# Kernel optimization log

Measured on AMD Instinct MI355X. Metric: run time of the kernel, lower is better.

Reference implementation:

```python
import jax, jax.numpy as jnp
import numpy as np

N_NODES = 50000
N_EDGES = 800000
IN_DIM = 256
HID = 64
LAT = 64
HEADS = 4
NUM_GRAPHS = 64
NEG_SLOPE = 0.2


def _gat_layer(h_in, src, dst, W, a_s, a_d, b, heads, concat):
    N = h_in.shape[0]
    F_ = W.shape[1] // heads
    h = (h_in @ W).reshape(N, heads, F_)              # [N,H,F]
    al_s = jnp.sum(h * a_s, axis=-1)                  # [N,H]
    al_d = jnp.sum(h * a_d, axis=-1)                  # [N,H]
    e = jax.nn.leaky_relu(al_s[src] + al_d[dst], NEG_SLOPE)  # [E,H]
    # scatter-softmax over edges grouped by destination node
    m = jax.ops.segment_max(e, dst, num_segments=N)
    e = jnp.exp(e - m[dst])
    s = jax.ops.segment_sum(e, dst, num_segments=N)
    alpha = e / (s[dst] + 1e-16)                      # [E,H]
    out = jax.ops.segment_sum(h[src] * alpha[:, :, None], dst, num_segments=N)
    out = out.reshape(N, heads * F_) if concat else out.mean(axis=1)
    return out + b


def setup_inputs() -> dict:
    key = jax.random.key(0)
    ks = jax.random.split(key, 20)
    g = lambda k, shp, sc: jax.random.normal(k, shp, jnp.float32) * sc
    inp = {}
    inp['x'] = g(ks[0], (N_NODES, IN_DIM), 1.0)
    inp['edge_index'] = jax.random.randint(ks[1], (2, N_EDGES), 0, N_NODES, jnp.int32)
    inp['batch'] = jnp.sort(jax.random.randint(ks[2], (N_NODES,), 0, NUM_GRAPHS, jnp.int32))
    # layer 0: IN_DIM -> HID, 4 heads, concat
    inp['W1'] = g(ks[3], (IN_DIM, HEADS * HID), 0.05)
    inp['a1s'] = g(ks[4], (HEADS, HID), 0.05)
    inp['a1d'] = g(ks[5], (HEADS, HID), 0.05)
    inp['b1'] = jnp.zeros((HEADS * HID,), jnp.float32)
    # layer 1: 4*HID -> HID, 4 heads, concat
    inp['W2'] = g(ks[6], (HEADS * HID, HEADS * HID), 0.05)
    inp['a2s'] = g(ks[7], (HEADS, HID), 0.05)
    inp['a2d'] = g(ks[8], (HEADS, HID), 0.05)
    inp['b2'] = jnp.zeros((HEADS * HID,), jnp.float32)
    # layer 2: 4*HID -> LAT, 1 head, mean
    inp['W3'] = g(ks[9], (HEADS * HID, LAT), 0.05)
    inp['a3s'] = g(ks[10], (1, LAT), 0.05)
    inp['a3d'] = g(ks[11], (1, LAT), 0.05)
    inp['b3'] = jnp.zeros((LAT,), jnp.float32)
    # VAE head
    inp['Wmu'] = g(ks[12], (LAT, LAT), 0.1)
    inp['bmu'] = jnp.zeros((LAT,), jnp.float32)
    inp['Wlv'] = g(ks[13], (LAT, LAT), 0.1)
    inp['blv'] = jnp.zeros((LAT,), jnp.float32)
    return inp


def reference(x, edge_index, batch, W1, a1s, a1d, b1, W2, a2s, a2d, b2,
              W3, a3s, a3d, b3, Wmu, bmu, Wlv, blv):
    N = x.shape[0]
    loop = jnp.arange(N, dtype=edge_index.dtype)
    src = jnp.concatenate([edge_index[0], loop])   # add self-loops (PyG default)
    dst = jnp.concatenate([edge_index[1], loop])
    h = _gat_layer(x, src, dst, W1, a1s, a1d, b1, HEADS, True)
    h = jax.nn.elu(h)
    h = _gat_layer(h, src, dst, W2, a2s, a2d, b2, HEADS, True)
    h = jax.nn.elu(h)
    h = _gat_layer(h, src, dst, W3, a3s, a3d, b3, 1, False)
    # global mean pool per graph
    sums = jax.ops.segment_sum(h, batch, num_segments=NUM_GRAPHS)
    cnts = jax.ops.segment_sum(jnp.ones((N,), h.dtype), batch, num_segments=NUM_GRAPHS)
    pooled = sums / jnp.maximum(cnts, 1.0)[:, None]  # [G, LAT]
    mu = pooled @ Wmu + bmu
    logvar = pooled @ Wlv + blv
    std = jnp.exp(0.5 * logvar)
    eps = jax.random.normal(jax.random.key(42), std.shape, std.dtype)
    z = mu + eps * std
    return (mu, logvar, z)
```

## Files before the change

kernel.cpp:

```cpp
#include <hip/hip_runtime.h>
#include <hip/hip_bf16.h>
#include <cstdint>
#include <math.h>


#define N_NODES 50000
#define N_EDGES 800000
#define NEG_SLOPE 0.2f
#define CAP 128
#define WTB 192

typedef __hip_bfloat16 bf16;
typedef short short8 __attribute__((ext_vector_type(8)));
typedef float floatx4 __attribute__((ext_vector_type(4)));
typedef float floatx2 __attribute__((ext_vector_type(2)));

__device__ __forceinline__ float bf2f(bf16 v){ return __bfloat162float(v); }
__device__ __forceinline__ float bflo(unsigned u){ union{unsigned u; float f;} c; c.u = u<<16; return c.f; }
__device__ __forceinline__ float bfhi(unsigned u){ union{unsigned u; float f;} c; c.u = u & 0xFFFF0000u; return c.f; }
__device__ __forceinline__ float leaky(float v){ return v>0.f ? v : NEG_SLOPE*v; }
__device__ __forceinline__ unsigned short f2bu(float f){
  union{ bf16 b; unsigned short u; } c; c.b = __float2bfloat16(f); return c.u;
}
__device__ __forceinline__ unsigned char f2fp8(float v){
  int p = __builtin_amdgcn_cvt_pk_fp8_f32(v, v, 0, false);
  return (unsigned char)(p & 0xff);
}
__device__ __forceinline__ void acc_fp8x4(float* acc, unsigned wrd, float wgt){
  floatx2 lo = __builtin_amdgcn_cvt_pk_f32_fp8((int)wrd, false);
  floatx2 hi = __builtin_amdgcn_cvt_pk_f32_fp8((int)wrd, true);
  acc[0] = fmaf(lo[0], wgt, acc[0]);
  acc[1] = fmaf(lo[1], wgt, acc[1]);
  acc[2] = fmaf(hi[0], wgt, acc[2]);
  acc[3] = fmaf(hi[1], wgt, acc[3]);
}

__device__ __forceinline__ void tf_round(unsigned& x0, unsigned& x1, int r){
  x0 += x1; x1 = (x1<<r)|(x1>>(32-r)); x1 ^= x0;
}
__device__ __forceinline__ void threefry2x32(unsigned k0, unsigned k1, unsigned& x0, unsigned& x1){
  unsigned ks2 = k0 ^ k1 ^ 0x1BD11BDAu;
  x0 += k0; x1 += k1;
  tf_round(x0,x1,13); tf_round(x0,x1,15); tf_round(x0,x1,26); tf_round(x0,x1,6);
  x0 += k1; x1 += ks2 + 1u;
  tf_round(x0,x1,17); tf_round(x0,x1,29); tf_round(x0,x1,16); tf_round(x0,x1,24);
  x0 += ks2; x1 += k0 + 2u;
  tf_round(x0,x1,13); tf_round(x0,x1,15); tf_round(x0,x1,26); tf_round(x0,x1,6);
  x0 += k0; x1 += k1 + 3u;
  tf_round(x0,x1,17); tf_round(x0,x1,29); tf_round(x0,x1,16); tf_round(x0,x1,24);
  x0 += k1; x1 += ks2 + 4u;
  tf_round(x0,x1,13); tf_round(x0,x1,15); tf_round(x0,x1,26); tf_round(x0,x1,6);
  x0 += ks2; x1 += k0 + 5u;
}

__device__ __forceinline__ float erfinv_approx(float x){
  float w = -log1pf(-x*x);
  float p;
  if (w < 5.0f){
    w = w - 2.5f;
    p = 2.81022636e-08f;
    p = fmaf(p,w,3.43273939e-07f);
    p = fmaf(p,w,-3.5233877e-06f);
    p = fmaf(p,w,-4.39150654e-06f);
    p = fmaf(p,w,0.00021858087f);
    p = fmaf(p,w,-0.00125372503f);
    p = fmaf(p,w,-0.00417768164f);
    p = fmaf(p,w,0.246640727f);
    p = fmaf(p,w,1.50140941f);
  } else {
    w = sqrtf(w) - 3.0f;
    p = -0.000200214257f;
    p = fmaf(p,w,0.000100950558f);
    p = fmaf(p,w,0.00134934322f);
    p = fmaf(p,w,-0.00367342844f);
    p = fmaf(p,w,0.00573950773f);
    p = fmaf(p,w,-0.0076224613f);
    p = fmaf(p,w,0.00943887047f);
    p = fmaf(p,w,1.00167406f);
    p = fmaf(p,w,2.83297682f);
  }
  return p*x;
}

__global__ __launch_bounds__(256) void wt_build_kernel(
        const float* __restrict__ W1, const float* __restrict__ W2,
        const float* __restrict__ W3, short* __restrict__ Wt1,
        short* __restrict__ Wt2, short* __restrict__ Wt3,
        const int* __restrict__ ei, int* __restrict__ deg,
        unsigned short* __restrict__ csr){
  __shared__ float tile[32][33];
  const int bx = (int)blockIdx.x;
  if (bx < WTB){
    const int z = bx >> 6, rem = bx & 63;
    const int gx = rem & 7, gy = rem >> 3;
    const float* W; short* Wt; int Nn;
    if (z == 0){ W = W1; Wt = Wt1; Nn = 256; }
    else if (z == 1){ W = W2; Wt = Wt2; Nn = 256; }
    else { W = W3; Wt = Wt3; Nn = 64; }
    const int n0 = gx*32, k0 = gy*32;
    if (n0 >= Nn) return;
    const int tx = threadIdx.x & 31, ty = threadIdx.x >> 5;
    #pragma unroll
    for (int i=0;i<4;++i)
      tile[ty+8*i][tx] = W[(size_t)(k0+ty+8*i)*Nn + n0 + tx];
    __syncthreads();
    #pragma unroll
    for (int i=0;i<4;++i)
      Wt[(size_t)(n0+ty+8*i)*256 + k0 + tx] = (short)f2bu(tile[tx][ty+8*i]);
  } else {
    int idx = (bx - WTB)*256 + (int)threadIdx.x;
    if (idx < N_EDGES + N_NODES){
      int s_ = (idx < N_EDGES) ? ei[idx]          : idx - N_EDGES;
      int d_ = (idx < N_EDGES) ? ei[N_EDGES+idx]  : idx - N_EDGES;
      int r = atomicAdd(&deg[d_], 1);
      if (r < CAP) csr[(size_t)d_*CAP + r] = (unsigned short)s_;
    }
  }
}

template<int OUT, bool INBF>
__global__ __launch_bounds__(256) void gemm_mfma_kernel(const void* __restrict__ inp,
        const short* __restrict__ Wt, void* __restrict__ outv,
        const float* __restrict__ a_s, const float* __restrict__ a_d,
        float* __restrict__ als, float* __restrict__ ald, int N){
  constexpr int M_BLK = (OUT==256) ? 64 : 256;
  constexpr int H = (OUT==256) ? 4 : 1;
  __shared__ short As[M_BLK*48];
  __shared__ short Bs[OUT*48];
  const int t = threadIdx.x;
  const int w = t>>6, lane = t&63;
  const int lm = lane&15, g = lane>>4;
  const int m0 = blockIdx.x * M_BLK;
  const int m_off = (OUT==256) ? 0 : w*64;
  const int n0    = (OUT==256) ? w*64 : 0;

  floatx4 acc[4][4] = {};

  for (int kk=0; kk<8; ++kk){
    const int k0 = kk*32;
    __syncthreads();
    for (int a = t; a < M_BLK*4; a += 256){
      int r = a>>2, c = a&3;
      int gr = m0 + r;
      uint4 v = make_uint4(0u,0u,0u,0u);
      if (gr < N){
        if constexpr (INBF){
          v = *(const uint4*)((const bf16*)inp + (size_t)gr*256 + k0 + c*8);
        } else {
          const float* p = (const float*)inp + (size_t)gr*256 + k0 + c*8;
          float4 f0 = *(const float4*)p;
          float4 f1 = *(const float4*)(p+4);
          v.x = (unsigned)f2bu(f0.x) | ((unsigned)f2bu(f0.y)<<16);
          v.y = (unsigned)f2bu(f0.z) | ((unsigned)f2bu(f0.w)<<16);
          v.z = (unsigned)f2bu(f1.x) | ((unsigned)f2bu(f1.y)<<16);
          v.w = (unsigned)f2bu(f1.z) | ((unsigned)f2bu(f1.w)<<16);
        }
      }
      *(uint4*)&As[r*48 + c*8] = v;
    }
    for (int a = t; a < OUT*4; a += 256){
      int r = a>>2, c = a&3;
      uint4 v = *(const uint4*)(Wt + (size_t)r*256 + k0 + c*8);
      *(uint4*)&Bs[r*48 + c*8] = v;
    }
    __syncthreads();
    short8 af[4], bfr[4];
    #pragma unroll
    for (int mt=0;mt<4;++mt)
      af[mt] = *(const short8*)&As[(m_off + mt*16 + lm)*48 + g*8];
    #pragma unroll
    for (int nt=0;nt<4;++nt)
      bfr[nt] = *(const short8*)&Bs[(n0 + nt*16 + lm)*48 + g*8];
    #pragma unroll
    for (int mt=0;mt<4;++mt)
      #pragma unroll
      for (int nt=0;nt<4;++nt)
        acc[mt][nt] = __builtin_amdgcn_mfma_f32_16x16x32_bf16(af[mt], bfr[nt], acc[mt][nt], 0, 0, 0);
  }

  float asv[4], adv[4];
  #pragma unroll
  for (int nt=0;nt<4;++nt){
    asv[nt] = a_s[n0 + nt*16 + lm];
    adv[nt] = a_d[n0 + nt*16 + lm];
  }
  const int head = (OUT==256) ? w : 0;
  #pragma unroll
  for (int mt=0;mt<4;++mt){
    #pragma unroll
    for (int reg=0;reg<4;++reg){
      int gr = m0 + m_off + mt*16 + g*4 + reg;
      bool valid = gr < N;
      float ps = 0.f, pd = 0.f;
      #pragma unroll
      for (int nt=0;nt<4;++nt){
        float v = acc[mt][nt][reg];
        if (valid){
          ((unsigned char*)outv)[(size_t)gr*OUT + n0 + nt*16 + lm] = f2fp8(v);
        }
        ps = fmaf(v, asv[nt], ps);
        pd = fmaf(v, adv[nt], pd);
      }
      #pragma unroll
      for (int o=1;o<16;o<<=1){ ps += __shfl_xor(ps,o); pd += __shfl_xor(pd,o); }
      if (lm==0 && valid){
        als[gr*H + head] = ps;
        ald[gr*H + head] = pd;
      }
    }
  }
}

template<bool ELU>
__global__ __launch_bounds__(256) void aggregate4_kernel(const unsigned char* __restrict__ h8,
        const float* __restrict__ als, const float* __restrict__ ald,
        const int* __restrict__ deg, const unsigned short* __restrict__ csr,
        const float* __restrict__ bias, bf16* __restrict__ out){
  __shared__ int   s_src[4][64];
  __shared__ float s_w[4][64][4];
  const int wv_ = threadIdx.x >> 6;
  const int n = blockIdx.x*4 + wv_;
  if (n >= N_NODES) return;
  const int lane = threadIdx.x & 63;
  const int r = lane>>4;
  const int f = lane&15;
  const int head = f>>2;
  const int p0 = n*CAP;
  const int cnt = min(deg[n], CAP);
  const float4 aldn4 = *(const float4*)(ald + n*4);
  float ssum = 0.f;
  float acc[16] = {};
  for (int c=0; c<cnt; c+=64){
    int e = c + lane;
    int src = n; float4 w4 = make_float4(0.f,0.f,0.f,0.f);
    if (e < cnt){
      src = (int)csr[p0+e];
      float4 av = *(const float4*)(als + src*4);
      w4.x = expf(leaky(av.x + aldn4.x));
      w4.y = expf(leaky(av.y + aldn4.y));
      w4.z = expf(leaky(av.z + aldn4.z));
      w4.w = expf(leaky(av.w + aldn4.w));
    }
    s_src[wv_][lane] = src;
    *(float4*)&s_w[wv_][lane][0] = w4;
    int ce = min(64, cnt - c);
    int cp = (ce+7)&~7;
    for (int i=0;i<cp;i+=8){
      int src0 = s_src[wv_][i+r], src1 = s_src[wv_][i+4+r];
      float w0 = s_w[wv_][i+r][head], w1 = s_w[wv_][i+4+r][head];
      uint4 h0 = *(const uint4*)(h8 + (size_t)src0*256 + f*16);
      uint4 h1 = *(const uint4*)(h8 + (size_t)src1*256 + f*16);
      ssum += w0 + w1;
      acc_fp8x4(acc+0,  h0.x, w0); acc_fp8x4(acc+4,  h0.y, w0);
      acc_fp8x4(acc+8,  h0.z, w0); acc_fp8x4(acc+12, h0.w, w0);
      acc_fp8x4(acc+0,  h1.x, w1); acc_fp8x4(acc+4,  h1.y, w1);
      acc_fp8x4(acc+8,  h1.z, w1); acc_fp8x4(acc+12, h1.w, w1);
    }
  }
  #pragma unroll
  for (int j=0;j<16;++j){
    acc[j] += __shfl_xor(acc[j], 16);
    acc[j] += __shfl_xor(acc[j], 32);
  }
  ssum += __shfl_xor(ssum, 16);
  ssum += __shfl_xor(ssum, 32);
  if (r==0){
    float inv = 1.f/(ssum + 1e-16f);
    #pragma unroll
    for (int half=0; half<2; ++half){
      float4 b0 = *(const float4*)(bias + f*16 + half*8);
      float4 b1 = *(const float4*)(bias + f*16 + half*8 + 4);
      float rv[8];
      rv[0]=acc[half*8+0]*inv+b0.x; rv[1]=acc[half*8+1]*inv+b0.y;
      rv[2]=acc[half*8+2]*inv+b0.z; rv[3]=acc[half*8+3]*inv+b0.w;
      rv[4]=acc[half*8+4]*inv+b1.x; rv[5]=acc[half*8+5]*inv+b1.y;
      rv[6]=acc[half*8+6]*inv+b1.z; rv[7]=acc[half*8+7]*inv+b1.w;
      union{ bf16 b[8]; uint4 u; } pk;
      #pragma unroll
      for (int j=0;j<8;++j){
        float v = rv[j];
        if (ELU) v = (v>0.f)?v:expm1f(v);
        pk.b[j] = __float2bfloat16(v);
      }
      *(uint4*)(out + (size_t)n*256 + f*16 + half*8) = pk.u;
    }
  }
}

__global__ __launch_bounds__(256) void aggregate1_kernel(const unsigned char* __restrict__ h8,
        const float* __restrict__ als, const float* __restrict__ ald,
        const int* __restrict__ deg, const unsigned short* __restrict__ csr,
        const float* __restrict__ bias, bf16* __restrict__ out){
  __shared__ int   s_src[4][64];
  __shared__ float s_w[4][64];
  const int wv_ = threadIdx.x >> 6;
  const int n = blockIdx.x*4 + wv_;
  if (n >= N_NODES) return;
  const int lane = threadIdx.x & 63;
  const int r = lane>>4;
  const int f = lane&15;
  const int p0 = n*CAP;
  const int cnt = min(deg[n], CAP);
  const float aldn = ald[n];
  float ssum = 0.f;
  float acc[4] = {};
  for (int c=0; c<cnt; c+=64){
    int e = c + lane;
    int src = n; float wv = 0.f;
    if (e < cnt){
      src = (int)csr[p0+e];
      wv = expf(leaky(als[src] + aldn));
    }
    s_src[wv_][lane] = src; s_w[wv_][lane] = wv;
    int ce = min(64, cnt - c);
    int cp = (ce+7)&~7;
    for (int i=0;i<cp;i+=8){
      int src0 = s_src[wv_][i+r], src1 = s_src[wv_][i+4+r];
      float w0 = s_w[wv_][i+r],   w1 = s_w[wv_][i+4+r];
      unsigned h0 = *(const unsigned*)(h8 + (size_t)src0*64 + f*4);
      unsigned h1 = *(const unsigned*)(h8 + (size_t)src1*64 + f*4);
      ssum += w0 + w1;
      acc_fp8x4(acc, h0, w0);
      acc_fp8x4(acc, h1, w1);
    }
  }
  #pragma unroll
  for (int j=0;j<4;++j){
    acc[j] += __shfl_xor(acc[j], 16);
    acc[j] += __shfl_xor(acc[j], 32);
  }
  ssum += __shfl_xor(ssum, 16);
  ssum += __shfl_xor(ssum, 32);
  if (r==0){
    float inv = 1.f/(ssum + 1e-16f);
    union{ bf16 b[4]; uint2 u; } pk;
    #pragma unroll
    for (int j=0;j<4;++j) pk.b[j] = __float2bfloat16(acc[j]*inv + bias[f*4+j]);
    *(uint2*)(out + (size_t)n*64 + f*4) = pk.u;
  }
}

__global__ __launch_bounds__(64) void pool_kernel(const bf16* __restrict__ h3,
        const int* __restrict__ batch, float* __restrict__ psum, float* __restrict__ pcnt,
        int N, int chunk){
  int n0 = blockIdx.x*chunk;
  if (n0 >= N) return;
  int n1 = min(N, n0+chunk);
  int t = threadIdx.x;
  int gcur = batch[n0];
  float acc = 0.f, cnt = 0.f;
  for (int n=n0; n<n1; ++n){
    int g = batch[n];
    if (g != gcur){
      atomicAdd(&psum[gcur*64+t], acc);
      if (t==0) atomicAdd(&pcnt[gcur], cnt);
      acc = 0.f; cnt = 0.f; gcur = g;
    }
    acc += bf2f(h3[(size_t)n*64+t]);
    cnt += 1.f;
  }
  atomicAdd(&psum[gcur*64+t], acc);
  if (t==0) atomicAdd(&pcnt[gcur], cnt);
}

__global__ __launch_bounds__(64) void head_kernel(const float* __restrict__ psum,
        const float* __restrict__ pcnt,
        const float* __restrict__ Wmu, const float* __restrict__ bmu,
        const float* __restrict__ Wlv, const float* __restrict__ blv,
        float* __restrict__ out){
  int g = blockIdx.x, t = threadIdx.x;
  __shared__ float p[64];
  float cnt = fmaxf(pcnt[g], 1.0f);
  p[t] = psum[g*64+t] / cnt;
  __syncthreads();
  float mu = bmu[t], lv = blv[t];
  for (int k=0;k<64;++k){
    float pk = p[k];
    mu = fmaf(pk, Wmu[(size_t)k*64+t], mu);
    lv = fmaf(pk, Wlv[(size_t)k*64+t], lv);
  }
  int i = g*64 + t;
  unsigned x0 = 0u, x1 = (unsigned)i;
  threefry2x32(0u, 42u, x0, x1);
  unsigned bits = x0 ^ x1;
  float f = __uint_as_float((bits>>9) | 0x3F800000u) - 1.0f;
  const float lo = __uint_as_float(0xBF7FFFFFu);
  float u = fmaxf(lo, f*2.0f + lo);
  float eps = 1.41421356f * erfinv_approx(u);
  float z = mu + eps * expf(0.5f*lv);
  out[i]        = mu;
  out[4096 + i] = lv;
  out[8192 + i] = z;
}

extern "C" void kernel_launch(void* const* d_in, const int* in_sizes, int n_in,
                              void* d_out, int out_size, void* d_ws, size_t ws_size,
                              hipStream_t stream){
  const float* x    = (const float*)d_in[0];
  const int*   ei   = (const int*)d_in[1];
  const int*   batch= (const int*)d_in[2];
  const float* W1   = (const float*)d_in[3];
  const float* a1s  = (const float*)d_in[4];
  const float* a1d  = (const float*)d_in[5];
  const float* b1   = (const float*)d_in[6];
  const float* W2   = (const float*)d_in[7];
  const float* a2s  = (const float*)d_in[8];
  const float* a2d  = (const float*)d_in[9];
  const float* b2   = (const float*)d_in[10];
  const float* W3   = (const float*)d_in[11];
  const float* a3s  = (const float*)d_in[12];
  const float* a3d  = (const float*)d_in[13];
  const float* b3   = (const float*)d_in[14];
  const float* Wmu  = (const float*)d_in[15];
  const float* bmu  = (const float*)d_in[16];
  const float* Wlv  = (const float*)d_in[17];
  const float* blv  = (const float*)d_in[18];
  float* out = (float*)d_out;

  const int N = N_NODES, E = N_EDGES;
  const int ET = E + N;

  char* ws = (char*)d_ws;
  size_t o = 0;
  auto alloc = [&](size_t bytes)->void*{
    void* p = ws + o; o += (bytes + 255) & ~(size_t)255; return p;
  };
  bf16*  hA      = (bf16*) alloc((size_t)N*256*2);
  unsigned char* hB8 = (unsigned char*)alloc((size_t)N*256);
  unsigned char* h38 = (unsigned char*)alloc((size_t)N*64);
  float* als     = (float*)alloc((size_t)N*4*4);
  float* ald     = (float*)alloc((size_t)N*4*4);
  const size_t degBytes  = ((size_t)N*4 + 255) & ~(size_t)255;
  const size_t poolBytes = 64*64*4 + 64*4;
  int*   deg     = (int*)  alloc((size_t)N*4);
  float* psum    = (float*)alloc(poolBytes);
  float* pcnt    = psum + 64*64;
  unsigned short* csr16 = (unsigned short*)alloc((size_t)N*CAP*2);
  short* Wt1     = (short*)alloc(256*256*2);
  short* Wt2     = (short*)alloc(256*256*2);
  short* Wt3     = (short*)alloc(64*256*2);
  (void)ws_size; (void)n_in; (void)in_sizes; (void)out_size;

  hipMemsetAsync(deg, 0, degBytes + poolBytes, stream);

  const int buildBlocks = (ET + 255)/256;
  wt_build_kernel<<<WTB + buildBlocks, 256, 0, stream>>>(
      W1, W2, W3, Wt1, Wt2, Wt3, ei, deg, csr16);

  gemm_mfma_kernel<256,false><<<(N+63)/64, 256, 0, stream>>>(x, Wt1, hB8, a1s, a1d, als, ald, N);
  aggregate4_kernel<true><<<(N+3)/4, 256, 0, stream>>>(hB8, als, ald, deg, csr16, b1, hA);

  gemm_mfma_kernel<256,true><<<(N+63)/64, 256, 0, stream>>>(hA, Wt2, hB8, a2s, a2d, als, ald, N);
  aggregate4_kernel<true><<<(N+3)/4, 256, 0, stream>>>(hB8, als, ald, deg, csr16, b2, hA);

  gemm_mfma_kernel<64,true><<<(N+255)/256, 256, 0, stream>>>(hA, Wt3, h38, a3s, a3d, als, ald, N);
  aggregate1_kernel<<<(N+3)/4, 256, 0, stream>>>(h38, als, ald, deg, csr16, b3, hA);

  const int PBLK = 512;
  const int chunk = (N + PBLK - 1)/PBLK;
  pool_kernel<<<PBLK, 64, 0, stream>>>(hA, batch, psum, pcnt, N, chunk);
  head_kernel<<<64, 64, 0, stream>>>(psum, pcnt, Wmu, bmu, Wlv, blv, out);
}
```

Baseline: 417.9 us.

## Fuse layer-1 GEMM with CSR build into one launch; split weight transpose

```diff
diff --git a/kernel.cpp b/kernel.cpp
--- a/kernel.cpp
+++ b/kernel.cpp
@@ -8,7 +8,7 @@
 #define N_EDGES 800000
 #define NEG_SLOPE 0.2f
 #define CAP 128
-#define WTB 192
+#define GB1 ((N_NODES+63)/64)
 
 typedef __hip_bfloat16 bf16;
 typedef short short8 __attribute__((ext_vector_type(8)));
@@ -82,38 +82,113 @@
   return p*x;
 }
 
-__global__ __launch_bounds__(256) void wt_build_kernel(
+__global__ __launch_bounds__(256) void wt_all_kernel(
         const float* __restrict__ W1, const float* __restrict__ W2,
         const float* __restrict__ W3, short* __restrict__ Wt1,
-        short* __restrict__ Wt2, short* __restrict__ Wt3,
+        short* __restrict__ Wt2, short* __restrict__ Wt3){
+  const float* W; short* Wt; int Nn;
+  if (blockIdx.z == 0){ W = W1; Wt = Wt1; Nn = 256; }
+  else if (blockIdx.z == 1){ W = W2; Wt = Wt2; Nn = 256; }
+  else { W = W3; Wt = Wt3; Nn = 64; }
+  const int n0 = blockIdx.x*32, k0 = blockIdx.y*32;
+  if (n0 >= Nn) return;
+  __shared__ float tile[32][33];
+  const int tx = threadIdx.x & 31, ty = threadIdx.x >> 5;
+  #pragma unroll
+  for (int i=0;i<4;++i)
+    tile[ty+8*i][tx] = W[(size_t)(k0+ty+8*i)*Nn + n0 + tx];
+  __syncthreads();
+  #pragma unroll
+  for (int i=0;i<4;++i)
+    Wt[(size_t)(n0+ty+8*i)*256 + k0 + tx] = (short)f2bu(tile[tx][ty+8*i]);
+}
+
+__global__ __launch_bounds__(256) void fused_g1b_kernel(
+        const float* __restrict__ x, const short* __restrict__ Wt1,
+        unsigned char* __restrict__ hB8,
+        const float* __restrict__ a1s, const float* __restrict__ a1d,
+        float* __restrict__ als, float* __restrict__ ald,
         const int* __restrict__ ei, int* __restrict__ deg,
         unsigned short* __restrict__ csr){
-  __shared__ float tile[32][33];
+  __shared__ short As[64*48];
   const int bx = (int)blockIdx.x;
-  if (bx < WTB){
-    const int z = bx >> 6, rem = bx & 63;
-    const int gx = rem & 7, gy = rem >> 3;
-    const float* W; short* Wt; int Nn;
-    if (z == 0){ W = W1; Wt = Wt1; Nn = 256; }
-    else if (z == 1){ W = W2; Wt = Wt2; Nn = 256; }
-    else { W = W3; Wt = Wt3; Nn = 64; }
-    const int n0 = gx*32, k0 = gy*32;
-    if (n0 >= Nn) return;
-    const int tx = threadIdx.x & 31, ty = threadIdx.x >> 5;
-    #pragma unroll
-    for (int i=0;i<4;++i)
-      tile[ty+8*i][tx] = W[(size_t)(k0+ty+8*i)*Nn + n0 + tx];
-    __syncthreads();
-    #pragma unroll
-    for (int i=0;i<4;++i)
-      Wt[(size_t)(n0+ty+8*i)*256 + k0 + tx] = (short)f2bu(tile[tx][ty+8*i]);
-  } else {
-    int idx = (bx - WTB)*256 + (int)threadIdx.x;
+  if (bx >= GB1){
+    int idx = (bx - GB1)*256 + (int)threadIdx.x;
     if (idx < N_EDGES + N_NODES){
       int s_ = (idx < N_EDGES) ? ei[idx]          : idx - N_EDGES;
       int d_ = (idx < N_EDGES) ? ei[N_EDGES+idx]  : idx - N_EDGES;
       int r = atomicAdd(&deg[d_], 1);
       if (r < CAP) csr[(size_t)d_*CAP + r] = (unsigned short)s_;
+    }
+    return;
+  }
+  const int t = threadIdx.x;
+  const int w = t>>6, lane = t&63;
+  const int lm = lane&15, g = lane>>4;
+  const int m0 = bx * 64;
+  const int n0 = w*64;
+
+  floatx4 acc[4][4] = {};
+
+  for (int kk=0; kk<8; ++kk){
+    const int k0 = kk*32;
+    __syncthreads();
+    for (int a = t; a < 64*4; a += 256){
+      int r = a>>2, c = a&3;
+      int gr = m0 + r;
+      uint4 v = make_uint4(0u,0u,0u,0u);
+      if (gr < N_NODES){
+        const float* p = x + (size_t)gr*256 + k0 + c*8;
+        float4 f0 = *(const float4*)p;
+        float4 f1 = *(const float4*)(p+4);
+        v.x = (unsigned)f2bu(f0.x) | ((unsigned)f2bu(f0.y)<<16);
+        v.y = (unsigned)f2bu(f0.z) | ((unsigned)f2bu(f0.w)<<16);
+        v.z = (unsigned)f2bu(f1.x) | ((unsigned)f2bu(f1.y)<<16);
+        v.w = (unsigned)f2bu(f1.z) | ((unsigned)f2bu(f1.w)<<16);
+      }
+      *(uint4*)&As[r*48 + c*8] = v;
+    }
+    __syncthreads();
+    short8 af[4], bfr[4];
+    #pragma unroll
+    for (int mt=0;mt<4;++mt)
+      af[mt] = *(const short8*)&As[(mt*16 + lm)*48 + g*8];
+    #pragma unroll
+    for (int nt=0;nt<4;++nt)
+      bfr[nt] = *(const short8*)(Wt1 + (size_t)(n0 + nt*16 + lm)*256 + k0 + g*8);
+    #pragma unroll
+    for (int mt=0;mt<4;++mt)
+      #pragma unroll
+      for (int nt=0;nt<4;++nt)
+        acc[mt][nt] = __builtin_amdgcn_mfma_f32_16x16x32_bf16(af[mt], bfr[nt], acc[mt][nt], 0, 0, 0);
+  }
+
+  float asv[4], adv[4];
+  #pragma unroll
+  for (int nt=0;nt<4;++nt){
+    asv[nt] = a1s[n0 + nt*16 + lm];
+    adv[nt] = a1d[n0 + nt*16 + lm];
+  }
+  #pragma unroll
+  for (int mt=0;mt<4;++mt){
+    #pragma unroll
+    for (int reg=0;reg<4;++reg){
+      int gr = m0 + mt*16 + g*4 + reg;
+      bool valid = gr < N_NODES;
+      float ps = 0.f, pd = 0.f;
+      #pragma unroll
+      for (int nt=0;nt<4;++nt){
+        float v = acc[mt][nt][reg];
+        if (valid) hB8[(size_t)gr*256 + n0 + nt*16 + lm] = f2fp8(v);
+        ps = fmaf(v, asv[nt], ps);
+        pd = fmaf(v, adv[nt], pd);
+      }
+      #pragma unroll
+      for (int o=1;o<16;o<<=1){ ps += __shfl_xor(ps,o); pd += __shfl_xor(pd,o); }
+      if (lm==0 && valid){
+        als[gr*4 + w] = ps;
+        ald[gr*4 + w] = pd;
+      }
     }
   }
 }
@@ -443,11 +518,11 @@
 
   hipMemsetAsync(deg, 0, degBytes + poolBytes, stream);
 
+  wt_all_kernel<<<dim3(8,8,3), 256, 0, stream>>>(W1, W2, W3, Wt1, Wt2, Wt3);
+
   const int buildBlocks = (ET + 255)/256;
-  wt_build_kernel<<<WTB + buildBlocks, 256, 0, stream>>>(
-      W1, W2, W3, Wt1, Wt2, Wt3, ei, deg, csr16);
-
-  gemm_mfma_kernel<256,false><<<(N+63)/64, 256, 0, stream>>>(x, Wt1, hB8, a1s, a1d, als, ald, N);
+  fused_g1b_kernel<<<GB1 + buildBlocks, 256, 0, stream>>>(
+      x, Wt1, hB8, a1s, a1d, als, ald, ei, deg, csr16);
   aggregate4_kernel<true><<<(N+3)/4, 256, 0, stream>>>(hB8, als, ald, deg, csr16, b1, hA);
 
   gemm_mfma_kernel<256,true><<<(N+63)/64, 256, 0, stream>>>(hA, Wt2, hB8, a2s, a2d, als, ald, N);
```

Result: no change. 421.8 us (+0.9%).
